# Performance work log

Measured on AMD Instinct MI355X. Metric: run time of the kernel, lower is better.

Reference implementation:

```python
import jax, jax.numpy as jnp
import numpy as np

BATCH = 250
SEQ = 200
EMB = 100
VOCAB = 100000
UNITS = 512


def setup_inputs() -> dict:
    key = jax.random.key(0)
    ks = jax.random.split(key, 12)
    s = 0.05
    return {
        "tokens": jax.random.randint(ks[0], (BATCH, SEQ), 0, VOCAB, dtype=jnp.int64 if jax.config.jax_enable_x64 else jnp.int32),
        "emb": jax.random.normal(ks[1], (VOCAB, EMB), jnp.float32) * s,
        "k0": jax.random.normal(ks[2], (EMB, 4 * UNITS), jnp.float32) * s,
        "r0": jax.random.normal(ks[3], (UNITS, 4 * UNITS), jnp.float32) * s,
        "b0": jnp.zeros((4 * UNITS,), jnp.float32),
        "k1": jax.random.normal(ks[4], (UNITS, 4 * UNITS), jnp.float32) * s,
        "r1": jax.random.normal(ks[5], (UNITS, 4 * UNITS), jnp.float32) * s,
        "b1": jnp.zeros((4 * UNITS,), jnp.float32),
        "wd1": jax.random.normal(ks[6], (UNITS, 32), jnp.float32) * s,
        "bd1": jnp.zeros((32,), jnp.float32),
        "wd2": jax.random.normal(ks[7], (32, 1), jnp.float32) * s,
        "bd2": jnp.zeros((1,), jnp.float32),
    }


def _lstm_step(x, h, c, k, r, b):
    # Keras LSTMCell gate order: [i, f, cbar, o]
    g = x @ k + h @ r + b  # [B, 4U]
    i, f, cbar, o = jnp.split(g, 4, axis=-1)
    c_new = jax.nn.sigmoid(f) * c + jax.nn.sigmoid(i) * jnp.tanh(cbar)
    h_new = jax.nn.sigmoid(o) * jnp.tanh(c_new)
    return h_new, c_new


def reference(tokens, emb, k0, r0, b0, k1, r1, b1, wd1, bd1, wd2, bd2):
    x = emb[tokens]  # [B, T, E]
    B = x.shape[0]
    U = r0.shape[0]

    def step(carry, xt):
        h0, c0, h1, c1 = carry
        h0, c0 = _lstm_step(xt, h0, c0, k0, r0, b0)
        h1, c1 = _lstm_step(h0, h1, c1, k1, r1, b1)
        return (h0, c0, h1, c1), None

    init = tuple(jnp.zeros((B, U), x.dtype) for _ in range(4))
    (h0, c0, h1, c1), _ = jax.lax.scan(step, init, jnp.swapaxes(x, 0, 1))
    prob = jax.nn.sigmoid((h1 @ wd1 + bd1) @ wd2 + bd2)  # [B, 1]
    return prob
```

## Files before the change

### kernel.cpp

```cpp
#include <hip/hip_runtime.h>
#include <cstdint>

typedef unsigned short u16;
typedef __attribute__((ext_vector_type(8))) short s8v;
typedef __attribute__((ext_vector_type(4))) float f4v;
typedef __attribute__((ext_vector_type(16))) float f16v;

#define TSEQ 200
#define HSLOT (256 * 512)

__device__ __forceinline__ u16 f2bf(float f) {
  uint32_t u = __float_as_uint(f);
  u += 0x7fffu + ((u >> 16) & 1u);
  return (u16)(u >> 16);
}
__device__ __forceinline__ float bf2f(u16 h) {
  return __uint_as_float(((uint32_t)h) << 16);
}
__device__ __forceinline__ float sigf(float x) { return 1.f / (1.f + __expf(-x)); }
__device__ __forceinline__ float tanhfast(float x) { return 2.f / (1.f + __expf(-2.f * x)) - 1.f; }

__device__ __forceinline__ void ld_c(s8v& d, const u16* p, int ofs) {
  asm volatile("global_load_dwordx4 %0, %1, off offset:%2 sc0 sc1"
               : "=v"(d) : "v"(p), "n"(ofs));
}
__device__ __forceinline__ void ld_nc(s8v& d, const u16* p, int ofs) {
  asm volatile("global_load_dwordx4 %0, %1, off offset:%2"
               : "=v"(d) : "v"(p), "n"(ofs));
}
__device__ __forceinline__ void vmwait(int n) {
  asm volatile("s_waitcnt vmcnt(%0)" :: "n"(n) : "memory");
}
__device__ __forceinline__ void cstore(u16* p, u16 v) {
  asm volatile("global_store_short %0, %1, off sc0 sc1" :: "v"(p), "v"((uint32_t)v) : "memory");
}


__global__ void zero_ws(uint32_t* p, int n) {
  int i = blockIdx.x * 256 + threadIdx.x;
  if (i < n) p[i] = 0u;
}

__global__ void gather_x(const int* __restrict__ tokens, const float* __restrict__ emb,
                         u16* __restrict__ X) {
  int idx = blockIdx.x * 256 + threadIdx.x;
  if (idx >= TSEQ * 256 * 16) return;
  int e0 = (idx & 15) * 8;
  int b  = (idx >> 4) & 255;
  int t  = idx >> 12;
  u16 v[8];
  if (b < 250) {
    int tok = tokens[b * TSEQ + t];
    const float* er = emb + (size_t)tok * 100;
#pragma unroll
    for (int j = 0; j < 8; ++j) {
      int e = e0 + j;
      v[j] = (e < 100) ? f2bf(er[e]) : (u16)0;
    }
  } else {
#pragma unroll
    for (int j = 0; j < 8; ++j) v[j] = 0;
  }
  *(s8v*)&X[(size_t)idx * 8] = *(const s8v*)v;
}

__global__ void pack_wB(const float* __restrict__ A, const float* __restrict__ Bm,
                        u16* __restrict__ out, int nk16, int split, int arows) {
  int idx = blockIdx.x * 256 + threadIdx.x;
  int total = 32 * nk16 * 2 * 32 * 2;
  if (idx >= total) return;
  int kh = idx & 1;
  int col = (idx >> 1) & 31;
  int colt = (idx >> 6) & 1;
  int rest = idx >> 7;
  int ks = rest % nk16;
  int ub = rest / nk16;
  int gcol = (colt * 2 + (col >> 4)) * 512 + ub * 16 + (col & 15);
  u16 v[8];
#pragma unroll
  for (int e = 0; e < 8; ++e) {
    int k = ks * 16 + kh * 8 + e;
    float f;
    if (k < split) f = (k < arows) ? A[(size_t)k * 2048 + gcol] : 0.f;
    else           f = Bm[(size_t)(k - split) * 2048 + gcol];
    v[e] = f2bf(f);
  }
  *(s8v*)&out[(size_t)idx * 8] = *(const s8v*)v;
}

template <bool LH, int NS, int NK16, int NX>
__device__ __forceinline__ void run_layer(int band, int ub, int w, int lane, int tid,
    const u16* __restrict__ Wp, const u16* __restrict__ X,
    u16* __restrict__ H0, u16* __restrict__ H1,
    const float* __restrict__ bp, unsigned* fL0b, unsigned* fL1b, float* rbuf) {
  s8v B0[NS], B1[NS];
#pragma unroll
  for (int s = 0; s < NS; ++s) {
    const u16* bb = Wp + (size_t)(ub * NK16 + w * NS + s) * 1024
                       + ((lane & 31) * 2 + (lane >> 5)) * 8;
    B0[s] = *(const s8v*)bb;
    B1[s] = *(const s8v*)(bb + 512);
  }
  const int arow = band * 32 + (lane & 31);
  const int kchE = (lane >> 5) * 8;
  const int u0 = (tid * 2) & 15;
  float bias0[4], bias1[4];
#pragma unroll
  for (int g = 0; g < 4; ++g) {
    bias0[g] = bp[g * 512 + ub * 16 + u0];
    bias1[g] = bp[g * 512 + ub * 16 + u0 + 1];
  }
  float c0 = 0.f, c1 = 0.f;
  unsigned* pp; int tofs;
  if (LH) {
    if (w < 2) { pp = fL0b + (lane & 31); tofs = 1; }
    else       { pp = fL1b + (lane & 31); tofs = 0; }
  } else {
    pp = (lane < 32) ? (fL0b + lane) : (fL1b + (lane - 32));
    tofs = (lane < 32) ? 0 : -3;
  }
  unsigned* sigp = (LH ? fL1b : fL0b) + ub;

  for (int t = 0; t < TSEQ; ++t) {
    const int cs = t & 3, ps = (t + 3) & 3;
    {
      const int thr = t + tofs;
      unsigned v;
      do {
        v = __hip_atomic_load(pp, __ATOMIC_RELAXED, __HIP_MEMORY_SCOPE_AGENT);
      } while (!__all((int)v >= thr));
    }
    const u16 *pH, *pX;
    if (LH) {
      pH = (w < 2 ? H0 + (size_t)cs * HSLOT : H1 + (size_t)ps * HSLOT)
           + (size_t)arow * 512 + kchE + (w & 1) * 256;
      pX = pH;
    } else if (NX > 0) {
      pX = X + (size_t)t * 32768 + arow * 128 + kchE;
      pH = H0 + (size_t)ps * HSLOT + (size_t)arow * 512 + kchE - 128;
    } else {
      pH = H0 + (size_t)ps * HSLOT + (size_t)arow * 512 + kchE + (w * 10 - 8) * 16;
      pX = pH;
    }
    f16v acc0 = {}, acc1 = {};
    s8v a[NS];
    constexpr int W = NS < 8 ? NS : 8;
#pragma unroll
    for (int s = 0; s < W; ++s) {
      if (s < NX) ld_nc(a[s], pX, s * 32); else ld_c(a[s], pH, s * 32);
    }
#pragma unroll
    for (int s = 0; s < NS; ++s) {
      const int j = s + W;
      if (j < NS) { if (j < NX) ld_nc(a[j], pX, j * 32); else ld_c(a[j], pH, j * 32); }
      const int rem = NS - 1 - s;
      vmwait(rem < W ? rem : W);
      __builtin_amdgcn_sched_barrier(0);
      acc0 = __builtin_amdgcn_mfma_f32_32x32x16_bf16(a[s], B0[s], acc0, 0, 0, 0);
      acc1 = __builtin_amdgcn_mfma_f32_32x32x16_bf16(a[s], B1[s], acc1, 0, 0, 0);
    }
#pragma unroll
    for (int q = 0; q < 4; ++q) {
      f4v v0 = {acc0[4*q], acc0[4*q+1], acc0[4*q+2], acc0[4*q+3]};
      f4v v1 = {acc1[4*q], acc1[4*q+1], acc1[4*q+2], acc1[4*q+3]};
      *(f4v*)&rbuf[(w * 8 + q) * 256 + lane * 4] = v0;
      *(f4v*)&rbuf[(w * 8 + 4 + q) * 256 + lane * 4] = v1;
    }
    __syncthreads();
    u16* Hout = (LH ? H1 : H0) + (size_t)cs * HSLOT;
    {
      const int cell = tid * 2, row = cell >> 4, u = cell & 15;
      const int hi = (row >> 2) & 1, r = (row & 3) | ((row >> 3) << 2);
      float gs[4];
#pragma unroll
      for (int g = 0; g < 4; ++g) {
        const int dwb = ((g >> 1) * 4 + (r >> 2)) * 256 + (((g & 1) << 4) + u + (hi << 5)) * 4 + (r & 3);
        gs[g] = rbuf[dwb] + rbuf[dwb + 2048] + rbuf[dwb + 4096] + rbuf[dwb + 6144];
      }
      float cn = sigf(gs[1] + bias0[1]) * c0 + sigf(gs[0] + bias0[0]) * tanhfast(gs[2] + bias0[2]);
      c0 = cn;
      cstore(&Hout[(size_t)(band * 32 + row) * 512 + ub * 16 + u],
             f2bf(sigf(gs[3] + bias0[3]) * tanhfast(cn)));
    }
    {
      const int cell = tid * 2 + 1, row = cell >> 4, u = cell & 15;
      const int hi = (row >> 2) & 1, r = (row & 3) | ((row >> 3) << 2);
      float gs[4];
#pragma unroll
      for (int g = 0; g < 4; ++g) {
        const int dwb = ((g >> 1) * 4 + (r >> 2)) * 256 + (((g & 1) << 4) + u + (hi << 5)) * 4 + (r & 3);
        gs[g] = rbuf[dwb] + rbuf[dwb + 2048] + rbuf[dwb + 4096] + rbuf[dwb + 6144];
      }
      float cn = sigf(gs[1] + bias1[1]) * c1 + sigf(gs[0] + bias1[0]) * tanhfast(gs[2] + bias1[2]);
      c1 = cn;
      cstore(&Hout[(size_t)(band * 32 + row) * 512 + ub * 16 + u],
             f2bf(sigf(gs[3] + bias1[3]) * tanhfast(cn)));
    }
    vmwait(0);
    __syncthreads();
    if (tid == 0)
      __hip_atomic_store(sigp, (unsigned)(t + 1), __ATOMIC_RELAXED, __HIP_MEMORY_SCOPE_AGENT);
  }
}

__global__ void __launch_bounds__(256, 2)
lstm_main(const float* __restrict__ b0, const float* __restrict__ b1,
          const u16* __restrict__ W0p, const u16* __restrict__ W1p,
          const u16* __restrict__ X, u16* __restrict__ H0,
          u16* __restrict__ H1, unsigned* __restrict__ fL0,
          unsigned* __restrict__ fL1) {
  __shared__ float rbuf[8192];
  const int tid = threadIdx.x, lane = tid & 63, w = tid >> 6;
  const int blk = blockIdx.x;
  const bool Lh = blk >= 256;
  const int sub = blk & 255, band = sub >> 5, ub = sub & 31;
  unsigned* fL0b = fL0 + band * 32;
  unsigned* fL1b = fL1 + band * 32;
  if (Lh)
    run_layer<true, 16, 64, 0>(band, ub, w, lane, tid, W1p, X, H0, H1, b1, fL0b, fL1b, rbuf);
  else if (w == 0)
    run_layer<false, 10, 40, 8>(band, ub, w, lane, tid, W0p, X, H0, H1, b0, fL0b, fL1b, rbuf);
  else
    run_layer<false, 10, 40, 0>(band, ub, w, lane, tid, W0p, X, H0, H1, b0, fL0b, fL1b, rbuf);
}


__global__ void dense_out(const u16* __restrict__ H1f, const float* __restrict__ wd1,
                          const float* __restrict__ bd1, const float* __restrict__ wd2,
                          const float* __restrict__ bd2, float* __restrict__ out) {
  __shared__ float wv[512];
  __shared__ float beff;
  const int t = threadIdx.x;
  {
    float s = 0.f;
#pragma unroll 4
    for (int j = 0; j < 32; ++j) s += wd1[t * 32 + j] * wd2[j];
    wv[t] = s;
  }
  if (t == 0) {
    float sb = 0.f;
    for (int j = 0; j < 32; ++j) sb += bd1[j] * wd2[j];
    beff = sb + bd2[0];
  }
  __syncthreads();
  if (t < 250) {
    const u16* hr = H1f + (size_t)t * 512;
    float acc = 0.f;
    for (int u = 0; u < 512; u += 8) {
      s8v hv = *(const s8v*)&hr[u];
#pragma unroll
      for (int j = 0; j < 8; ++j) acc += bf2f((u16)hv[j]) * wv[u + j];
    }
    out[t] = sigf(acc + beff);
  }
}


extern "C" void kernel_launch(void* const* d_in, const int* in_sizes, int n_in,
                              void* d_out, int out_size, void* d_ws, size_t ws_size,
                              hipStream_t stream) {
  const int*   tokens = (const int*)  d_in[0];
  const float* emb    = (const float*)d_in[1];
  const float* k0     = (const float*)d_in[2];
  const float* r0     = (const float*)d_in[3];
  const float* b0     = (const float*)d_in[4];
  const float* k1     = (const float*)d_in[5];
  const float* r1     = (const float*)d_in[6];
  const float* b1     = (const float*)d_in[7];
  const float* wd1    = (const float*)d_in[8];
  const float* bd1    = (const float*)d_in[9];
  const float* wd2    = (const float*)d_in[10];
  const float* bd2    = (const float*)d_in[11];
  float* out = (float*)d_out;

  char* ws = (char*)d_ws;
  unsigned* fL0 = (unsigned*)ws;
  unsigned* fL1 = (unsigned*)(ws + 2048);
  u16* H0  = (u16*)(ws + 8192);
  u16* H1  = (u16*)(ws + 8192 + 1048576);
  u16* X   = (u16*)(ws + 8192 + 2097152);
  u16* W0p = (u16*)(ws + 8192 + 2097152 + 13107200);
  u16* W1p = (u16*)(ws + 8192 + 2097152 + 13107200 + 2621440);

  zero_ws<<<2056, 256, 0, stream>>>((uint32_t*)ws, 526336);
  gather_x<<<3200, 256, 0, stream>>>(tokens, emb, X);
  pack_wB<<<640,  256, 0, stream>>>(k0, r0, W0p, 40, 128, 100);
  pack_wB<<<1024, 256, 0, stream>>>(k1, r1, W1p, 64, 512, 512);

  void* args[] = {(void*)&b0, (void*)&b1, (void*)&W0p, (void*)&W1p,
                  (void*)&X,  (void*)&H0, (void*)&H1, (void*)&fL0, (void*)&fL1};
  (void)hipLaunchCooperativeKernel(reinterpret_cast<void*>(lstm_main),
                                   dim3(512), dim3(256), args, 0, stream);

  dense_out<<<1, 512, 0, stream>>>(H1 + (size_t)3 * HSLOT, wd1, bd1, wd2, bd2, out);
}
```

Measured before the change: 1.880 ms.

## Stream weights per step, relax cache bits, pack h stores, remap blocks to XCDs

The recurrent weight fragments are no longer held in registers for the whole sequence. They are streamed from global memory each step and pipelined alongside the activation loads, which frees registers at the cost of more memory traffic per step. The coherent loads and stores drop the sc0 bit and keep only sc1. Each thread's two hidden outputs are packed into one dword store instead of two short stores. Block indices are remapped so that blocks sharing a unit band sit on the same XCD, which is meant to improve L2 locality for H and the flags.

```diff
diff --git a/kernel.cpp b/kernel.cpp
--- a/kernel.cpp
+++ b/kernel.cpp
@@ -21,7 +21,7 @@
 __device__ __forceinline__ float tanhfast(float x) { return 2.f / (1.f + __expf(-2.f * x)) - 1.f; }
 
 __device__ __forceinline__ void ld_c(s8v& d, const u16* p, int ofs) {
-  asm volatile("global_load_dwordx4 %0, %1, off offset:%2 sc0 sc1"
+  asm volatile("global_load_dwordx4 %0, %1, off offset:%2 sc1"
                : "=v"(d) : "v"(p), "n"(ofs));
 }
 __device__ __forceinline__ void ld_nc(s8v& d, const u16* p, int ofs) {
@@ -31,8 +31,8 @@
 __device__ __forceinline__ void vmwait(int n) {
   asm volatile("s_waitcnt vmcnt(%0)" :: "n"(n) : "memory");
 }
-__device__ __forceinline__ void cstore(u16* p, u16 v) {
-  asm volatile("global_store_short %0, %1, off sc0 sc1" :: "v"(p), "v"((uint32_t)v) : "memory");
+__device__ __forceinline__ void cstore_d(u16* p, uint32_t v) {
+  asm volatile("global_store_dword %0, %1, off sc1" :: "v"(p), "v"(v) : "memory");
 }
 
 
@@ -88,19 +88,44 @@
   *(s8v*)&out[(size_t)idx * 8] = *(const s8v*)v;
 }
 
+template <int NS, int NX>
+__device__ __forceinline__ void pipew(const u16* pX, const u16* pH, const u16* pB,
+                                      f16v& acc0, f16v& acc1) {
+  s8v a[NS];
+#pragma unroll
+  for (int s = 0; s < NS; ++s) {
+    if (s < NX) ld_nc(a[s], pX, s * 32);
+    else        ld_c(a[s], pH, (s - NX) * 32);
+  }
+  constexpr int W = NS < 6 ? NS : 6;
+  s8v b0[NS], b1[NS];
+#pragma unroll
+  for (int j = 0; j < W; ++j) {
+    ld_nc(b0[j], pB + j * 1024, 0);
+    ld_nc(b1[j], pB + j * 1024, 1024);
+  }
+#pragma unroll
+  for (int s = 0; s < NS; ++s) {
+    const int j = s + W;
+    if (j < NS) {
+      ld_nc(b0[j], pB + j * 1024, 0);
+      ld_nc(b1[j], pB + j * 1024, 1024);
+    }
+    const int rem = NS - 1 - s;
+    vmwait(2 * (rem < W ? rem : W));
+    __builtin_amdgcn_sched_barrier(0);
+    acc0 = __builtin_amdgcn_mfma_f32_32x32x16_bf16(a[s], b0[s], acc0, 0, 0, 0);
+    acc1 = __builtin_amdgcn_mfma_f32_32x32x16_bf16(a[s], b1[s], acc1, 0, 0, 0);
+  }
+}
+
 template <bool LH, int NS, int NK16, int NX>
 __device__ __forceinline__ void run_layer(int band, int ub, int w, int lane, int tid,
     const u16* __restrict__ Wp, const u16* __restrict__ X,
     u16* __restrict__ H0, u16* __restrict__ H1,
     const float* __restrict__ bp, unsigned* fL0b, unsigned* fL1b, float* rbuf) {
-  s8v B0[NS], B1[NS];
-#pragma unroll
-  for (int s = 0; s < NS; ++s) {
-    const u16* bb = Wp + (size_t)(ub * NK16 + w * NS + s) * 1024
-                       + ((lane & 31) * 2 + (lane >> 5)) * 8;
-    B0[s] = *(const s8v*)bb;
-    B1[s] = *(const s8v*)(bb + 512);
-  }
+  const u16* pB = Wp + (size_t)(ub * NK16 + w * NS) * 1024
+                     + ((lane & 31) * 2 + (lane >> 5)) * 8;
   const int arow = band * 32 + (lane & 31);
   const int kchE = (lane >> 5) * 8;
   const int u0 = (tid * 2) & 15;
@@ -137,28 +162,13 @@
       pX = pH;
     } else if (NX > 0) {
       pX = X + (size_t)t * 32768 + arow * 128 + kchE;
-      pH = H0 + (size_t)ps * HSLOT + (size_t)arow * 512 + kchE - 128;
+      pH = H0 + (size_t)ps * HSLOT + (size_t)arow * 512 + kchE;
     } else {
       pH = H0 + (size_t)ps * HSLOT + (size_t)arow * 512 + kchE + (w * 10 - 8) * 16;
       pX = pH;
     }
     f16v acc0 = {}, acc1 = {};
-    s8v a[NS];
-    constexpr int W = NS < 8 ? NS : 8;
-#pragma unroll
-    for (int s = 0; s < W; ++s) {
-      if (s < NX) ld_nc(a[s], pX, s * 32); else ld_c(a[s], pH, s * 32);
-    }
-#pragma unroll
-    for (int s = 0; s < NS; ++s) {
-      const int j = s + W;
-      if (j < NS) { if (j < NX) ld_nc(a[j], pX, j * 32); else ld_c(a[j], pH, j * 32); }
-      const int rem = NS - 1 - s;
-      vmwait(rem < W ? rem : W);
-      __builtin_amdgcn_sched_barrier(0);
-      acc0 = __builtin_amdgcn_mfma_f32_32x32x16_bf16(a[s], B0[s], acc0, 0, 0, 0);
-      acc1 = __builtin_amdgcn_mfma_f32_32x32x16_bf16(a[s], B1[s], acc1, 0, 0, 0);
-    }
+    pipew<NS, NX>(pX, pH, pB, acc0, acc1);
 #pragma unroll
     for (int q = 0; q < 4; ++q) {
       f4v v0 = {acc0[4*q], acc0[4*q+1], acc0[4*q+2], acc0[4*q+3]};
@@ -168,34 +178,27 @@
     }
     __syncthreads();
     u16* Hout = (LH ? H1 : H0) + (size_t)cs * HSLOT;
-    {
-      const int cell = tid * 2, row = cell >> 4, u = cell & 15;
-      const int hi = (row >> 2) & 1, r = (row & 3) | ((row >> 3) << 2);
+    const int row = tid >> 3, u = (tid * 2) & 15;
+    const int hi = (row >> 2) & 1, r = (row & 3) | ((row >> 3) << 2);
+    u16 hv[2];
+    float cc[2] = {c0, c1};
+    const float* bb[2] = {bias0, bias1};
+#pragma unroll
+    for (int h = 0; h < 2; ++h) {
       float gs[4];
 #pragma unroll
       for (int g = 0; g < 4; ++g) {
-        const int dwb = ((g >> 1) * 4 + (r >> 2)) * 256 + (((g & 1) << 4) + u + (hi << 5)) * 4 + (r & 3);
+        const int dwb = ((g >> 1) * 4 + (r >> 2)) * 256
+                        + (((g & 1) << 4) + (u + h) + (hi << 5)) * 4 + (r & 3);
         gs[g] = rbuf[dwb] + rbuf[dwb + 2048] + rbuf[dwb + 4096] + rbuf[dwb + 6144];
       }
-      float cn = sigf(gs[1] + bias0[1]) * c0 + sigf(gs[0] + bias0[0]) * tanhfast(gs[2] + bias0[2]);
-      c0 = cn;
-      cstore(&Hout[(size_t)(band * 32 + row) * 512 + ub * 16 + u],
-             f2bf(sigf(gs[3] + bias0[3]) * tanhfast(cn)));
-    }
-    {
-      const int cell = tid * 2 + 1, row = cell >> 4, u = cell & 15;
-      const int hi = (row >> 2) & 1, r = (row & 3) | ((row >> 3) << 2);
-      float gs[4];
-#pragma unroll
-      for (int g = 0; g < 4; ++g) {
-        const int dwb = ((g >> 1) * 4 + (r >> 2)) * 256 + (((g & 1) << 4) + u + (hi << 5)) * 4 + (r & 3);
-        gs[g] = rbuf[dwb] + rbuf[dwb + 2048] + rbuf[dwb + 4096] + rbuf[dwb + 6144];
-      }
-      float cn = sigf(gs[1] + bias1[1]) * c1 + sigf(gs[0] + bias1[0]) * tanhfast(gs[2] + bias1[2]);
-      c1 = cn;
-      cstore(&Hout[(size_t)(band * 32 + row) * 512 + ub * 16 + u],
-             f2bf(sigf(gs[3] + bias1[3]) * tanhfast(cn)));
-    }
+      float cn = sigf(gs[1] + bb[h][1]) * cc[h] + sigf(gs[0] + bb[h][0]) * tanhfast(gs[2] + bb[h][2]);
+      cc[h] = cn;
+      hv[h] = f2bf(sigf(gs[3] + bb[h][3]) * tanhfast(cn));
+    }
+    c0 = cc[0]; c1 = cc[1];
+    cstore_d(&Hout[(size_t)(band * 32 + row) * 512 + ub * 16 + u],
+             (uint32_t)hv[0] | ((uint32_t)hv[1] << 16));
     vmwait(0);
     __syncthreads();
     if (tid == 0)
@@ -212,8 +215,10 @@
   __shared__ float rbuf[8192];
   const int tid = threadIdx.x, lane = tid & 63, w = tid >> 6;
   const int blk = blockIdx.x;
-  const bool Lh = blk >= 256;
-  const int sub = blk & 255, band = sub >> 5, ub = sub & 31;
+  const int xcd = blk & 7, q = blk >> 3;
+  const int ub = xcd * 4 + (q & 3);
+  const bool Lh = ((q >> 2) & 1) != 0;
+  const int band = q >> 3;
   unsigned* fL0b = fL0 + band * 32;
   unsigned* fL1b = fL1 + band * 32;
   if (Lh)
```

After: 2.495 ms. 32.7% more time.
